# Kernel tuning notes

Measured on AMD Instinct MI355X. Metric: run time of the kernel, lower is better.

## Reference

```python
import jax, jax.numpy as jnp
import numpy as np
from jax import lax

TAU_MEM = 100.0   # 1/0.01 default
V_LEAK = 0.0
V_TH = 1.0


def setup_inputs() -> dict:
    key = jax.random.key(0)
    k1, k2 = jax.random.split(key)
    B, T, F = 32, 128, 2048
    inp = jax.random.normal(k1, (B, T, F), dtype=jnp.float32)
    W = jax.random.normal(k2, (F, F), dtype=jnp.float32) * (1.0 / np.sqrt(F))
    b = jnp.zeros((F,), dtype=jnp.float32)
    return {"input": inp, "W": W, "b": b}


def _heaviside(x):
    return (x > 0).astype(x.dtype)


def reference(input, W, b):
    # time-distributed kernel: Linear applied to all timesteps at once
    gs = jnp.einsum('btn,mn->btm', input, W) + b  # [B, T, F]
    dt_over_tau = 1.0 / TAU_MEM

    def step(v, g):
        # Euler LIF update with delta (subtractive) reset
        v_new = v + dt_over_tau * ((V_LEAK - v) + g)
        z = _heaviside(v_new - V_TH)
        v_reset = v_new - z * V_TH
        return v_reset, z

    v0 = jnp.zeros(gs.shape[::2], dtype=gs.dtype)  # [B, F]
    _, zs = lax.scan(step, v0, jnp.moveaxis(gs, 1, 0))  # zs: [T, B, F]
    return jnp.moveaxis(zs, 0, 1)  # [B, T, F]
```

## Files before the change

### kernel.cpp

```cpp
#include <hip/hip_runtime.h>
#include <hip/hip_bf16.h>
#include <stdint.h>

#define Bdim 32
#define Tdim 128
#define Fdim 2048
#define Mdim (Bdim*Tdim)

#define BM 256
#define BN 128
#define BK 64
#define NT (Fdim/BK)

typedef __attribute__((ext_vector_type(8))) short bf16x8;
typedef __attribute__((ext_vector_type(4))) float f32x4;

__device__ inline unsigned short f2bf(float f) {
    union { float f; unsigned u; } x; x.f = f;
    unsigned r = (x.u + 0x7fffu + ((x.u >> 16) & 1u)) >> 16;
    return (unsigned short)r;
}

__global__ void convert_kernel(const float* __restrict__ A, const float* __restrict__ W,
                               unsigned short* __restrict__ a16, unsigned short* __restrict__ w16) {
    const int nA4 = (Mdim * Fdim) / 4;
    const int nW4 = (Fdim * Fdim) / 4;
    const int stride = gridDim.x * blockDim.x;
    for (int i = blockIdx.x * blockDim.x + threadIdx.x; i < nA4 + nW4; i += stride) {
        const float4* src; unsigned short* dst; int j;
        if (i < nA4) { src = (const float4*)A; dst = a16; j = i; }
        else         { src = (const float4*)W; dst = w16; j = i - nA4; }
        float4 v = src[j];
        ushort4 o;
        o.x = f2bf(v.x); o.y = f2bf(v.y); o.z = f2bf(v.z); o.w = f2bf(v.w);
        *(ushort4*)(dst + 4 * (size_t)j) = o;
    }
}

__global__ __launch_bounds__(512, 2) void gemm_fused_kernel(const unsigned short* __restrict__ A,
                                                            const unsigned short* __restrict__ Wm,
                                                            const float* __restrict__ bias,
                                                            float* __restrict__ Z) {
    __shared__ __align__(16) char smem[147456];

    const int tid = threadIdx.x;
    const int wid = tid >> 6, lane = tid & 63;
    const int wr = wid >> 1, wc = wid & 1;
    const int m0 = blockIdx.y * BM, n0 = blockIdx.x * BN;

    f32x4 acc[4][4];
#pragma unroll
    for (int i = 0; i < 4; i++)
#pragma unroll
        for (int j = 0; j < 4; j++) acc[i][j] = f32x4{0.f, 0.f, 0.f, 0.f};

    const int frow = lane & 15;
    const int lgrp = lane >> 4;

    auto stage = [&](int buf, int kt) {
        const int k0 = kt * BK;
        char* sAb = smem + buf * 49152;
        char* sBb = sAb + 32768;
#pragma unroll
        for (int j = 0; j < 4; ++j) {
            const int base = wid * 4096 + j * 1024;
            const int off  = base + lane * 16;
            const int row  = off >> 7;
            const int chk  = (off & 127) >> 4;
            const int scol = (chk ^ (row & 7)) << 3;
            const unsigned short* ga = A + (size_t)(m0 + row) * Fdim + k0 + scol;
            __builtin_amdgcn_global_load_lds(
                (const __attribute__((address_space(1))) void*)ga,
                (__attribute__((address_space(3))) void*)(sAb + base), 16, 0, 0);
        }
#pragma unroll
        for (int j = 0; j < 2; ++j) {
            const int base = wid * 2048 + j * 1024;
            const int off  = base + lane * 16;
            const int row  = off >> 7;
            const int chk  = (off & 127) >> 4;
            const int scol = (chk ^ (row & 7)) << 3;
            const unsigned short* gb = Wm + (size_t)(n0 + row) * Fdim + k0 + scol;
            __builtin_amdgcn_global_load_lds(
                (const __attribute__((address_space(1))) void*)gb,
                (__attribute__((address_space(3))) void*)(sBb + base), 16, 0, 0);
        }
    };

    stage(0, 0);
    stage(1, 1);

#pragma unroll 1
    for (int t = 0; t < NT; ++t) {
        if (t < NT - 1) asm volatile("s_waitcnt vmcnt(6)" ::: "memory");
        else            asm volatile("s_waitcnt vmcnt(0)" ::: "memory");
        __builtin_amdgcn_s_barrier();
        __builtin_amdgcn_sched_barrier(0);
        if (t + 2 < NT) stage((t + 2) % 3, t + 2);

        const unsigned short* sAc = (const unsigned short*)(smem + (t % 3) * 49152);
        const unsigned short* sBc = (const unsigned short*)(smem + (t % 3) * 49152 + 32768);
        bf16x8 af[2][4], bfr[2][4];
#pragma unroll
        for (int kk = 0; kk < 2; kk++) {
            const int chunk = kk * 4 + lgrp;
#pragma unroll
            for (int mi = 0; mi < 4; mi++) {
                const int r = wr * 64 + mi * 16 + frow;
                af[kk][mi] = *(const bf16x8*)(sAc + r * BK + ((chunk ^ (r & 7)) << 3));
            }
#pragma unroll
            for (int ni = 0; ni < 4; ni++) {
                const int r = wc * 64 + ni * 16 + frow;
                bfr[kk][ni] = *(const bf16x8*)(sBc + r * BK + ((chunk ^ (r & 7)) << 3));
            }
        }
#pragma unroll
        for (int kk = 0; kk < 2; kk++)
#pragma unroll
            for (int mi = 0; mi < 4; mi++)
#pragma unroll
                for (int ni = 0; ni < 4; ni++)
                    acc[mi][ni] = __builtin_amdgcn_mfma_f32_16x16x32_bf16(af[kk][mi], bfr[kk][ni], acc[mi][ni], 0, 0, 0);
    }

    __syncthreads();

    float* ct = (float*)smem;
#pragma unroll
    for (int mi = 0; mi < 4; mi++)
#pragma unroll
        for (int ni = 0; ni < 4; ni++) {
            const int r0 = wr * 64 + mi * 16 + (lane >> 4) * 4;
            const int c0 = wc * 64 + ni * 16 + (lane & 15);
#pragma unroll
            for (int r = 0; r < 4; r++) ct[(r0 + r) * 132 + c0] = acc[mi][ni][r];
        }
    __syncthreads();

    if (tid < 256) {
        const int sub  = tid >> 7;
        const int col  = tid & 127;
        const int gcol = n0 + col;
        const float bf = bias[gcol];
        float* outp = Z + (size_t)(m0 + sub * 128) * Fdim + gcol;
        float v = 0.f;
#pragma unroll 16
        for (int t = 0; t < Tdim; t++) {
            const float g = ct[(sub * 128 + t) * 132 + col] + bf;
            const float vn = v + 0.01f * ((0.0f - v) + g);
            const float z = (vn > 1.0f) ? 1.0f : 0.0f;
            v = vn - z;
            outp[(size_t)t * Fdim] = z;
        }
    }
}

__global__ void gemm_f32_naive(const float* __restrict__ A, const float* __restrict__ W,
                               float* __restrict__ C) {
    int col = blockIdx.x * blockDim.x + threadIdx.x;
    int row = blockIdx.y;
    float s = 0.f;
    for (int k = 0; k < Fdim; k++) s += A[(size_t)row * Fdim + k] * W[(size_t)col * Fdim + k];
    C[(size_t)row * Fdim + col] = s;
}

__global__ __launch_bounds__(256, 1) void lif_kernel(float* __restrict__ gs,
                                                     const float* __restrict__ bias) {
    int idx = blockIdx.x * blockDim.x + threadIdx.x;
    int b = idx >> 11, f = idx & (Fdim - 1);
    const float bf = bias[f];
    float* p = gs + (size_t)b * Tdim * Fdim + f;
    float v = 0.f;
#pragma unroll 16
    for (int t = 0; t < Tdim; t++) {
        float g = p[(size_t)t * Fdim] + bf;
        float vn = v + 0.01f * ((0.0f - v) + g);
        float z = (vn > 1.0f) ? 1.0f : 0.0f;
        v = vn - z;
        p[(size_t)t * Fdim] = z;
    }
}

extern "C" void kernel_launch(void* const* d_in, const int* in_sizes, int n_in,
                              void* d_out, int out_size, void* d_ws, size_t ws_size,
                              hipStream_t stream) {
    const float* inp  = (const float*)d_in[0];
    const float* W    = (const float*)d_in[1];
    const float* bias = (const float*)d_in[2];
    float* out = (float*)d_out;

    const size_t needA = (size_t)Mdim * Fdim * 2;
    const size_t needW = (size_t)Fdim * Fdim * 2;

    if (ws_size >= needA + needW) {
        unsigned short* a16 = (unsigned short*)d_ws;
        unsigned short* w16 = (unsigned short*)((char*)d_ws + needA);
        convert_kernel<<<2048, 256, 0, stream>>>(inp, W, a16, w16);
        dim3 grid(Fdim / BN, Mdim / BM);
        gemm_fused_kernel<<<grid, 512, 0, stream>>>(a16, w16, bias, out);
    } else {
        dim3 grid(Fdim / 256, Mdim);
        gemm_f32_naive<<<grid, 256, 0, stream>>>(inp, W, out);
        lif_kernel<<<(Bdim * Fdim) / 256, 256, 0, stream>>>(out, bias);
    }
}
```

Baseline: 134.3 us.

## Split K-tile into two halves interleaving async staging with MFMA and raising priority

The main loop now handles each K tile in two halves of 32. The next tile's global-to-LDS loads are split into two groups, each issued before one half's fragment reads and MFMAs, and a second barrier sits mid-iteration. MFMA sections are wrapped in s_setprio(1) to favour compute waves. The aim is better overlap of memory issue with matrix math and lower register pressure from smaller fragment arrays, at the cost of an extra barrier and explicit lgkmcnt waits per iteration.

```diff
diff --git a/kernel.cpp b/kernel.cpp
--- a/kernel.cpp
+++ b/kernel.cpp
@@ -57,13 +57,28 @@
     const int frow = lane & 15;
     const int lgrp = lane >> 4;
 
-    auto stage = [&](int buf, int kt) {
+    auto stageA = [&](int buf, int kt) {
+        const int k0 = kt * BK;
+        char* sAb = smem + buf * 49152;
+#pragma unroll
+        for (int j = 0; j < 3; ++j) {
+            const int base = wid * 4096 + j * 1024;
+            const int off  = base + lane * 16;
+            const int row  = off >> 7;
+            const int chk  = (off & 127) >> 4;
+            const int scol = (chk ^ (row & 7)) << 3;
+            const unsigned short* ga = A + (size_t)(m0 + row) * Fdim + k0 + scol;
+            __builtin_amdgcn_global_load_lds(
+                (const __attribute__((address_space(1))) void*)ga,
+                (__attribute__((address_space(3))) void*)(sAb + base), 16, 0, 0);
+        }
+    };
+    auto stageB = [&](int buf, int kt) {
         const int k0 = kt * BK;
         char* sAb = smem + buf * 49152;
         char* sBb = sAb + 32768;
-#pragma unroll
-        for (int j = 0; j < 4; ++j) {
-            const int base = wid * 4096 + j * 1024;
+        {
+            const int base = wid * 4096 + 3 * 1024;
             const int off  = base + lane * 16;
             const int row  = off >> 7;
             const int chk  = (off & 127) >> 4;
@@ -87,41 +102,64 @@
         }
     };
 
-    stage(0, 0);
-    stage(1, 1);
+    stageA(0, 0); stageB(0, 0);
+    stageA(1, 1); stageB(1, 1);
 
 #pragma unroll 1
     for (int t = 0; t < NT; ++t) {
+        const unsigned short* sAc = (const unsigned short*)(smem + (t % 3) * 49152);
+        const unsigned short* sBc = (const unsigned short*)(smem + (t % 3) * 49152 + 32768);
+
         if (t < NT - 1) asm volatile("s_waitcnt vmcnt(6)" ::: "memory");
         else            asm volatile("s_waitcnt vmcnt(0)" ::: "memory");
         __builtin_amdgcn_s_barrier();
         __builtin_amdgcn_sched_barrier(0);
-        if (t + 2 < NT) stage((t + 2) % 3, t + 2);
-
-        const unsigned short* sAc = (const unsigned short*)(smem + (t % 3) * 49152);
-        const unsigned short* sBc = (const unsigned short*)(smem + (t % 3) * 49152 + 32768);
-        bf16x8 af[2][4], bfr[2][4];
-#pragma unroll
-        for (int kk = 0; kk < 2; kk++) {
-            const int chunk = kk * 4 + lgrp;
-#pragma unroll
-            for (int mi = 0; mi < 4; mi++) {
-                const int r = wr * 64 + mi * 16 + frow;
-                af[kk][mi] = *(const bf16x8*)(sAc + r * BK + ((chunk ^ (r & 7)) << 3));
-            }
-#pragma unroll
-            for (int ni = 0; ni < 4; ni++) {
-                const int r = wc * 64 + ni * 16 + frow;
-                bfr[kk][ni] = *(const bf16x8*)(sBc + r * BK + ((chunk ^ (r & 7)) << 3));
-            }
-        }
-#pragma unroll
-        for (int kk = 0; kk < 2; kk++)
-#pragma unroll
-            for (int mi = 0; mi < 4; mi++)
-#pragma unroll
-                for (int ni = 0; ni < 4; ni++)
-                    acc[mi][ni] = __builtin_amdgcn_mfma_f32_16x16x32_bf16(af[kk][mi], bfr[kk][ni], acc[mi][ni], 0, 0, 0);
+        if (t + 2 < NT) stageA((t + 2) % 3, t + 2);
+
+        bf16x8 af[4], bfr[4];
+#pragma unroll
+        for (int mi = 0; mi < 4; mi++) {
+            const int r = wr * 64 + mi * 16 + frow;
+            af[mi] = *(const bf16x8*)(sAc + r * BK + (((lgrp) ^ (r & 7)) << 3));
+        }
+#pragma unroll
+        for (int ni = 0; ni < 4; ni++) {
+            const int r = wc * 64 + ni * 16 + frow;
+            bfr[ni] = *(const bf16x8*)(sBc + r * BK + (((lgrp) ^ (r & 7)) << 3));
+        }
+        asm volatile("s_waitcnt lgkmcnt(0)" ::: "memory");
+        __builtin_amdgcn_sched_barrier(0);
+        __builtin_amdgcn_s_setprio(1);
+#pragma unroll
+        for (int mi = 0; mi < 4; mi++)
+#pragma unroll
+            for (int ni = 0; ni < 4; ni++)
+                acc[mi][ni] = __builtin_amdgcn_mfma_f32_16x16x32_bf16(af[mi], bfr[ni], acc[mi][ni], 0, 0, 0);
+        __builtin_amdgcn_s_setprio(0);
+
+        __builtin_amdgcn_s_barrier();
+        __builtin_amdgcn_sched_barrier(0);
+        if (t + 2 < NT) stageB((t + 2) % 3, t + 2);
+
+#pragma unroll
+        for (int mi = 0; mi < 4; mi++) {
+            const int r = wr * 64 + mi * 16 + frow;
+            af[mi] = *(const bf16x8*)(sAc + r * BK + (((4 + lgrp) ^ (r & 7)) << 3));
+        }
+#pragma unroll
+        for (int ni = 0; ni < 4; ni++) {
+            const int r = wc * 64 + ni * 16 + frow;
+            bfr[ni] = *(const bf16x8*)(sBc + r * BK + (((4 + lgrp) ^ (r & 7)) << 3));
+        }
+        asm volatile("s_waitcnt lgkmcnt(0)" ::: "memory");
+        __builtin_amdgcn_sched_barrier(0);
+        __builtin_amdgcn_s_setprio(1);
+#pragma unroll
+        for (int mi = 0; mi < 4; mi++)
+#pragma unroll
+            for (int ni = 0; ni < 4; ni++)
+                acc[mi][ni] = __builtin_amdgcn_mfma_f32_16x16x32_bf16(af[mi], bfr[ni], acc[mi][ni], 0, 0, 0);
+        __builtin_amdgcn_s_setprio(0);
     }
 
     __syncthreads();
```

New measurement: 135.0 us. Within noise of the previous version (+0.5%).
